# Kernel tuning notes

Hardware: AMD Instinct MI355X
Metric: run time of the kernel (lower is better)

## Reference

```python
import jax, jax.numpy as jnp
import numpy as np

N = 50000
E = 600000


def gcn_conv(x, W, b, src, dst, n):
    # PyG GCNConv: h = x @ W; add self-loops; symmetric normalization; aggregate; + bias
    h = x @ W  # [N, out]
    deg = jnp.zeros((n,), h.dtype).at[dst].add(1.0) + 1.0  # self-loop included
    dinv = jax.lax.rsqrt(deg)  # deg >= 1, always finite
    coef = dinv[src] * dinv[dst]  # [E]
    msg = h[src] * coef[:, None]  # [E, out]  (the memory-bound gather)
    agg = jax.ops.segment_sum(msg, dst, num_segments=n)
    agg = agg + h * (dinv * dinv)[:, None]  # self-loop contribution
    return agg + b


def setup_inputs() -> dict:
    key = jax.random.key(0)
    ks = jax.random.split(key, 8)
    x = jax.random.normal(ks[0], (N, 128), dtype=jnp.float32)
    edge_index = jax.random.randint(ks[1], (2, E), 0, N, dtype=jnp.int64 if jax.config.jax_enable_x64 else jnp.int32)
    def glorot(k, fan_in, fan_out):
        s = jnp.sqrt(6.0 / (fan_in + fan_out))
        return jax.random.uniform(k, (fan_in, fan_out), jnp.float32, -s, s)
    W1 = glorot(ks[2], 128, 128)
    b1 = jnp.zeros((128,), jnp.float32)
    W2 = glorot(ks[3], 128, 64)
    b2 = jnp.zeros((64,), jnp.float32)
    W3 = glorot(ks[4], 64, 16)
    b3 = jnp.zeros((16,), jnp.float32)
    return {"x": x, "edge_index": edge_index, "W1": W1, "b1": b1, "W2": W2, "b2": b2, "W3": W3, "b3": b3}


def reference(x, edge_index, W1, b1, W2, b2, W3, b3):
    src, dst = edge_index[0], edge_index[1]
    n = x.shape[0]
    h = jax.nn.relu(gcn_conv(x, W1, b1, src, dst, n))
    h = jax.nn.relu(gcn_conv(h, W2, b2, src, dst, n))
    h = gcn_conv(h, W3, b3, src, dst, n)
    return h
```

## Files before the change

### kernel.cpp

```cpp
#include <hip/hip_runtime.h>
#include <hip/hip_fp16.h>
#include <type_traits>


typedef _Float16 f16x8 __attribute__((ext_vector_type(8)));
typedef float f32x4 __attribute__((ext_vector_type(4)));

#define CSR_CAP 32

__device__ inline float2 h2f(unsigned int u) {
  __half2 h = __builtin_bit_cast(__half2, u);
  return __half22float2(h);
}

__device__ inline void fma8h(float4& a0, float4& a1, const uint4& g, float w) {
  float2 f0 = h2f(g.x), f1 = h2f(g.y), f2 = h2f(g.z), f3 = h2f(g.w);
  a0.x = fmaf(f0.x, w, a0.x);
  a0.y = fmaf(f0.y, w, a0.y);
  a0.z = fmaf(f1.x, w, a0.z);
  a0.w = fmaf(f1.y, w, a0.w);
  a1.x = fmaf(f2.x, w, a1.x);
  a1.y = fmaf(f2.y, w, a1.y);
  a1.z = fmaf(f3.x, w, a1.z);
  a1.w = fmaf(f3.y, w, a1.w);
}

__device__ inline void add8h(float4& a0, float4& a1, const uint4& g) {
  float2 f0 = h2f(g.x), f1 = h2f(g.y), f2 = h2f(g.z), f3 = h2f(g.w);
  a0.x += f0.x; a0.y += f0.y; a0.z += f1.x; a0.w += f1.y;
  a1.x += f2.x; a1.y += f2.y; a1.z += f3.x; a1.w += f3.y;
}

__device__ inline unsigned int pack2h(float x, float y) {
  __half2 h = __floats2half2_rn(x, y);
  return __builtin_bit_cast(unsigned int, h);
}

__device__ inline uint2 pack4h(const float4& v) {
  uint2 r;
  r.x = pack2h(v.x, v.y);
  r.y = pack2h(v.z, v.w);
  return r;
}

template <int K, int F, typename TIN>
__global__ __launch_bounds__(512) void gemm_mfma(const TIN* __restrict__ A,
                                                 const float* __restrict__ W,
                                                 __half* __restrict__ C16, int n,
                                                 int nwaves,
                                                 const int* __restrict__ src,
                                                 const int* __restrict__ dst,
                                                 int* __restrict__ cur,
                                                 unsigned short* __restrict__ csr,
                                                 int E) {
  constexpr int KP = K + 8;
  constexpr int KS = K / 32;
  constexpr int NT = F / 16;

  __shared__ __half Ws[F * KP];

  int t = threadIdx.x;

  if (t >= 256) {
    __syncthreads();
    int base = blockIdx.x * 256 + (t - 256);
    int stride = gridDim.x * 256;
    for (int e0 = base; e0 < E; e0 += 4 * stride) {
      int d[4], s[4];
      bool v[4];
#pragma unroll
      for (int u = 0; u < 4; ++u) {
        int e = e0 + u * stride;
        v[u] = e < E;
        int ee = v[u] ? e : 0;
        d[u] = dst[ee];
        s[u] = src[ee];
      }
      int pos[4];
#pragma unroll
      for (int u = 0; u < 4; ++u)
        if (v[u]) pos[u] = atomicAdd(&cur[d[u]], 1);
#pragma unroll
      for (int u = 0; u < 4; ++u)
        if (v[u]) {
          int p = pos[u] >= CSR_CAP ? CSR_CAP - 1 : pos[u];
          csr[(size_t)d[u] * CSR_CAP + p] = (unsigned short)s[u];
        }
    }
    return;
  }

  for (int i = t; i < K * F; i += 256) {
    int kk = i / F, nn = i % F;
    Ws[nn * KP + kk] = __float2half(W[i]);
  }
  __syncthreads();

  int wave = blockIdx.x * 4 + (t >> 6);
  if (wave >= nwaves) return;
  int lane = t & 63;
  int m = lane & 15;
  int quad = lane >> 4;

  int arow = wave * 16 + m;
  if (arow >= n) arow = n - 1;

  f16x8 af[KS];
  if constexpr (std::is_same_v<TIN, float>) {
#pragma unroll
    for (int ks = 0; ks < KS; ++ks) {
      const float* p = A + (size_t)arow * K + ks * 32 + quad * 8;
      float4 lo = *(const float4*)p;
      float4 hi = *(const float4*)(p + 4);
      f16x8 a;
      a[0] = (_Float16)lo.x; a[1] = (_Float16)lo.y;
      a[2] = (_Float16)lo.z; a[3] = (_Float16)lo.w;
      a[4] = (_Float16)hi.x; a[5] = (_Float16)hi.y;
      a[6] = (_Float16)hi.z; a[7] = (_Float16)hi.w;
      af[ks] = a;
    }
  } else {
#pragma unroll
    for (int ks = 0; ks < KS; ++ks)
      af[ks] = *(const f16x8*)(const void*)&A[(size_t)arow * K + ks * 32 + quad * 8];
  }

  f32x4 acc[NT];
#pragma unroll
  for (int nt = 0; nt < NT; ++nt) acc[nt] = (f32x4){0.f, 0.f, 0.f, 0.f};
#pragma unroll
  for (int nt = 0; nt < NT; ++nt)
#pragma unroll
    for (int ks = 0; ks < KS; ++ks) {
      f16x8 b = *(const f16x8*)(const void*)&Ws[(nt * 16 + m) * KP + ks * 32 + quad * 8];
      acc[nt] = __builtin_amdgcn_mfma_f32_16x16x32_f16(af[ks], b, acc[nt], 0, 0, 0);
    }

  int rbase = wave * 16 + quad * 4;
#pragma unroll
  for (int nt = 0; nt < NT; ++nt)
#pragma unroll
    for (int r = 0; r < 4; ++r) {
      int rr = rbase + r;
      if (rr < n) C16[(size_t)rr * F + nt * 16 + m] = __float2half(acc[nt][r]);
    }
}

template <int K, int F, int CPL, int EU, bool PRE, bool SCOUT>
__global__ __launch_bounds__(512) void aggmm(
    const __half* __restrict__ hprev, const float* __restrict__ W,
    const float* __restrict__ bias, const int* __restrict__ cnt,
    const unsigned short* __restrict__ csr, __half* __restrict__ C16, int n) {
  constexpr int KP = K + 8;
  constexpr int KS = K / 32;
  constexpr int NT = F / 16;
  constexpr int RS = K / 8;
  static_assert(8 * CPL == RS, "chunk coverage (8 chunk-lanes per half)");

  __shared__ __half Ws[F * KP];
  __shared__ __half As[32 * KP];

  int t = threadIdx.x;
  for (int i = t; i < K * F; i += 512) {
    int kk = i / F, nn = i % F;
    Ws[nn * KP + kk] = __float2half(W[i]);
  }

  int wid = t >> 6;
  int lane = t & 63;
  int nb = blockIdx.x * 32;

  {
    int ng = lane >> 4;
    int sl = lane & 15;
    int half = sl >> 3;
    int fl = sl & 7;
    int nib = wid * 4 + ng;
    int node = nb + nib;
    int nd = node < n ? node : n - 1;
    const uint4* h4 = (const uint4*)hprev;
    int c0 = cnt[nd];
    float di = rsqrtf((float)c0 + 1.0f);
    int cc = c0 < CSR_CAP ? c0 : CSR_CAP;
    float4 acc[CPL][2];
#pragma unroll
    for (int c = 0; c < CPL; ++c) {
      acc[c][0] = make_float4(0.f, 0.f, 0.f, 0.f);
      acc[c][1] = make_float4(0.f, 0.f, 0.f, 0.f);
    }
    if (half == 0) {
#pragma unroll
      for (int c = 0; c < CPL; ++c) {
        uint4 sv = h4[(size_t)nd * RS + fl + c * 8];
        if constexpr (PRE)
          add8h(acc[c][0], acc[c][1], sv);
        else
          fma8h(acc[c][0], acc[c][1], sv, di * di);
      }
    }
    int j0 = nd * CSR_CAP;
    int e = j0 + cc;
    int j = j0 + half;
    int p[EU];
#pragma unroll
    for (int u = 0; u < EU; ++u) p[u] = csr[j + 2 * u];
    for (; j + 2 * EU - 2 < e;) {
      uint4 g[EU][CPL];
#pragma unroll
      for (int u = 0; u < EU; ++u)
#pragma unroll
        for (int c = 0; c < CPL; ++c) g[u][c] = h4[(size_t)p[u] * RS + fl + c * 8];
      int cs[EU];
      if constexpr (!PRE) {
#pragma unroll
        for (int u = 0; u < EU; ++u) cs[u] = cnt[p[u]];
      }
      j += 2 * EU;
      int pn[EU];
#pragma unroll
      for (int u = 0; u < EU; ++u) pn[u] = csr[j + 2 * u];
#pragma unroll
      for (int u = 0; u < EU; ++u) {
        if constexpr (PRE) {
#pragma unroll
          for (int c = 0; c < CPL; ++c) add8h(acc[c][0], acc[c][1], g[u][c]);
        } else {
          float w = rsqrtf((float)cs[u] + 1.0f) * di;
#pragma unroll
          for (int c = 0; c < CPL; ++c) fma8h(acc[c][0], acc[c][1], g[u][c], w);
        }
      }
#pragma unroll
      for (int u = 0; u < EU; ++u) p[u] = pn[u];
    }
#pragma unroll
    for (int u = 0; u < EU; ++u) {
      if (j + 2 * u < e) {
        if constexpr (PRE) {
#pragma unroll
          for (int c = 0; c < CPL; ++c) {
            uint4 g = h4[(size_t)p[u] * RS + fl + c * 8];
            add8h(acc[c][0], acc[c][1], g);
          }
        } else {
          float w = rsqrtf((float)cnt[p[u]] + 1.0f) * di;
#pragma unroll
          for (int c = 0; c < CPL; ++c) {
            uint4 g = h4[(size_t)p[u] * RS + fl + c * 8];
            fma8h(acc[c][0], acc[c][1], g, w);
          }
        }
      }
    }
#pragma unroll
    for (int c = 0; c < CPL; ++c) {
      acc[c][0].x += __shfl_xor(acc[c][0].x, 8);
      acc[c][0].y += __shfl_xor(acc[c][0].y, 8);
      acc[c][0].z += __shfl_xor(acc[c][0].z, 8);
      acc[c][0].w += __shfl_xor(acc[c][0].w, 8);
      acc[c][1].x += __shfl_xor(acc[c][1].x, 8);
      acc[c][1].y += __shfl_xor(acc[c][1].y, 8);
      acc[c][1].z += __shfl_xor(acc[c][1].z, 8);
      acc[c][1].w += __shfl_xor(acc[c][1].w, 8);
    }
    if (half == 0) {
      float sc = PRE ? di : 1.0f;
#pragma unroll
      for (int c = 0; c < CPL; ++c) {
        int ch = fl + c * 8;
        float4 b0 = *(const float4*)&bias[ch * 8];
        float4 b1 = *(const float4*)&bias[ch * 8 + 4];
        float4 r0 = make_float4(fmaxf(acc[c][0].x * sc + b0.x, 0.f),
                                fmaxf(acc[c][0].y * sc + b0.y, 0.f),
                                fmaxf(acc[c][0].z * sc + b0.z, 0.f),
                                fmaxf(acc[c][0].w * sc + b0.w, 0.f));
        float4 r1 = make_float4(fmaxf(acc[c][1].x * sc + b1.x, 0.f),
                                fmaxf(acc[c][1].y * sc + b1.y, 0.f),
                                fmaxf(acc[c][1].z * sc + b1.z, 0.f),
                                fmaxf(acc[c][1].w * sc + b1.w, 0.f));
        uint2 lo = pack4h(r0), hi = pack4h(r1);
        uint4 pk;
        pk.x = lo.x; pk.y = lo.y; pk.z = hi.x; pk.w = hi.y;
        *(uint4*)&As[(size_t)nib * KP + ch * 8] = pk;
      }
    }
  }

  __syncthreads();

  if (wid < 2) {
    int m = lane & 15;
    int quad = lane >> 4;
    const __half* At = &As[(size_t)wid * 16 * KP];
    f16x8 af[KS];
#pragma unroll
    for (int ks = 0; ks < KS; ++ks)
      af[ks] = *(const f16x8*)(const void*)&At[m * KP + ks * 32 + quad * 8];

    f32x4 acc2[NT];
#pragma unroll
    for (int nt = 0; nt < NT; ++nt) acc2[nt] = (f32x4){0.f, 0.f, 0.f, 0.f};
#pragma unroll
    for (int nt = 0; nt < NT; ++nt)
#pragma unroll
      for (int ks = 0; ks < KS; ++ks) {
        f16x8 bfr = *(const f16x8*)(const void*)&Ws[(nt * 16 + m) * KP + ks * 32 + quad * 8];
        acc2[nt] = __builtin_amdgcn_mfma_f32_16x16x32_f16(af[ks], bfr, acc2[nt], 0, 0, 0);
      }

    int rbase = nb + wid * 16 + quad * 4;
    float rw[4];
#pragma unroll
    for (int r = 0; r < 4; ++r) {
      if constexpr (SCOUT) {
        int rr = rbase + r;
        int rc = rr < n ? rr : n - 1;
        rw[r] = rsqrtf((float)cnt[rc] + 1.0f);
      } else {
        rw[r] = 1.0f;
      }
    }
#pragma unroll
    for (int nt = 0; nt < NT; ++nt)
#pragma unroll
      for (int r = 0; r < 4; ++r) {
        int rr = rbase + r;
        if (rr < n) C16[(size_t)rr * F + nt * 16 + m] = __float2half(acc2[nt][r] * rw[r]);
      }
  }
}

__global__ __launch_bounds__(256) void agg_final(
    const __half* __restrict__ h16, const int* __restrict__ cnt,
    const unsigned short* __restrict__ csr, const float* __restrict__ bias,
    float* __restrict__ out, int n) {
  int node = blockIdx.x * 64 + threadIdx.x / 4;
  int q = threadIdx.x & 3;
  int half = q >> 1;
  int fl = q & 1;
  bool valid = node < n;
  int nd = valid ? node : n - 1;

  const uint4* h4 = (const uint4*)h16;
  int c0 = cnt[nd];
  float di = rsqrtf((float)c0 + 1.0f);
  int cc = c0 < CSR_CAP ? c0 : CSR_CAP;
  float4 a0 = make_float4(0.f, 0.f, 0.f, 0.f);
  float4 a1 = make_float4(0.f, 0.f, 0.f, 0.f);
  if (half == 0) {
    uint4 sv = h4[(size_t)nd * 2 + fl];
    add8h(a0, a1, sv);
  }
  int s = nd * CSR_CAP;
  int e = s + cc;
  int j = s + half;
  for (; j + 2 < e; j += 4) {
    int p0 = csr[j];
    int p1 = csr[j + 2];
    uint4 g0 = h4[(size_t)p0 * 2 + fl];
    uint4 g1 = h4[(size_t)p1 * 2 + fl];
    add8h(a0, a1, g0);
    add8h(a0, a1, g1);
  }
  for (; j < e; j += 2) {
    int p = csr[j];
    uint4 g = h4[(size_t)p * 2 + fl];
    add8h(a0, a1, g);
  }

  a0.x += __shfl_xor(a0.x, 2);
  a0.y += __shfl_xor(a0.y, 2);
  a0.z += __shfl_xor(a0.z, 2);
  a0.w += __shfl_xor(a0.w, 2);
  a1.x += __shfl_xor(a1.x, 2);
  a1.y += __shfl_xor(a1.y, 2);
  a1.z += __shfl_xor(a1.z, 2);
  a1.w += __shfl_xor(a1.w, 2);

  if (valid && half == 0) {
    float4 b0 = *(const float4*)&bias[fl * 8];
    float4 b1 = *(const float4*)&bias[fl * 8 + 4];
    float4 r0 = make_float4(a0.x * di + b0.x, a0.y * di + b0.y,
                            a0.z * di + b0.z, a0.w * di + b0.w);
    float4 r1 = make_float4(a1.x * di + b1.x, a1.y * di + b1.y,
                            a1.z * di + b1.z, a1.w * di + b1.w);
    float* op = &out[(size_t)node * 16 + fl * 8];
    *(float4*)op = r0;
    *(float4*)(op + 4) = r1;
  }
}


extern "C" void kernel_launch(void* const* d_in, const int* in_sizes, int n_in,
                              void* d_out, int out_size, void* d_ws, size_t ws_size,
                              hipStream_t stream) {
  const float* x = (const float*)d_in[0];
  const int* edge = (const int*)d_in[1];
  const float* W1 = (const float*)d_in[2];
  const float* b1 = (const float*)d_in[3];
  const float* W2 = (const float*)d_in[4];
  const float* b2 = (const float*)d_in[5];
  const float* W3 = (const float*)d_in[6];
  const float* b3 = (const float*)d_in[7];

  const int N = in_sizes[0] / 128;
  const int E = in_sizes[1] / 2;
  const int* src = edge;
  const int* dstp = edge + E;
  float* out = (float*)d_out;

  size_t off = 0;
  auto take = [&](size_t bytes) -> void* {
    void* r = (char*)d_ws + off;
    off += (bytes + 255) & ~(size_t)255;
    return r;
  };
  int* cur = (int*)take((size_t)N * 4);
  unsigned short* csr =
      (unsigned short*)take((size_t)N * CSR_CAP * 2 + 256);
  __half* t1 = (__half*)take((size_t)N * 128 * 2);
  __half* t2 = (__half*)take((size_t)N * 64 * 2);
  __half* t3 = (__half*)take((size_t)N * 16 * 2);

  hipMemsetAsync(d_ws, 0, ((size_t)N * 4 + 255) & ~(size_t)255, stream);

  int nwaves = (N + 15) / 16;
  int gblk = (nwaves + 3) / 4;
  int ablk = (N + 31) / 32;
  int fblk = (N + 63) / 64;

  gemm_mfma<128, 128, float><<<gblk, 512, 0, stream>>>(x, W1, t1, N, nwaves,
                                                       src, dstp, cur, csr, E);

  aggmm<128, 64, 2, 4, false, true><<<ablk, 512, 0, stream>>>(t1, W2, b1, cur, csr, t2, N);
  aggmm<64, 16, 1, 4, true, true><<<ablk, 512, 0, stream>>>(t2, W3, b2, cur, csr, t3, N);
  agg_final<<<fblk, 256, 0, stream>>>(t3, cur, csr, b3, out, N);
}
```

Baseline: 175.7 us.

## Process 64 nodes per block with 8 lanes per node and column passes

Each aggregation block now handles 64 nodes instead of 32. Each node gets 8 lanes instead of 16, so every lane walks the neighbour list in several sequential 32-column passes rather than holding all columns at once. Four waves run the MFMA epilogue instead of two, and the grid is halved. This cuts per-lane register pressure and raises concurrent nodes per wave, but the CSR indices and degree counts are now reread on every pass, and each gather covers fewer columns.

Result: slower. 186.5 us (+6.1%).

```diff
diff --git a/kernel.cpp b/kernel.cpp
--- a/kernel.cpp
+++ b/kernel.cpp
@@ -146,7 +146,7 @@
     }
 }
 
-template <int K, int F, int CPL, int EU, bool PRE, bool SCOUT>
+template <int K, int F, int P, int EU, bool PRE, bool SCOUT>
 __global__ __launch_bounds__(512) void aggmm(
     const __half* __restrict__ hprev, const float* __restrict__ W,
     const float* __restrict__ bias, const int* __restrict__ cnt,
@@ -155,10 +155,10 @@
   constexpr int KS = K / 32;
   constexpr int NT = F / 16;
   constexpr int RS = K / 8;
-  static_assert(8 * CPL == RS, "chunk coverage (8 chunk-lanes per half)");
+  static_assert(P * 32 == K, "chunk coverage (32 cols per pass)");
 
   __shared__ __half Ws[F * KP];
-  __shared__ __half As[32 * KP];
+  __shared__ __half As[64 * KP];
 
   int t = threadIdx.x;
   for (int i = t; i < K * F; i += 512) {
@@ -168,127 +168,108 @@
 
   int wid = t >> 6;
   int lane = t & 63;
-  int nb = blockIdx.x * 32;
+  int nb = blockIdx.x * 64;
 
   {
-    int ng = lane >> 4;
-    int sl = lane & 15;
-    int half = sl >> 3;
-    int fl = sl & 7;
-    int nib = wid * 4 + ng;
+    int ng = lane >> 3;
+    int sl = lane & 7;
+    int half = sl >> 2;
+    int fl = sl & 3;
+    int nib = wid * 8 + ng;
     int node = nb + nib;
     int nd = node < n ? node : n - 1;
     const uint4* h4 = (const uint4*)hprev;
     int c0 = cnt[nd];
     float di = rsqrtf((float)c0 + 1.0f);
     int cc = c0 < CSR_CAP ? c0 : CSR_CAP;
-    float4 acc[CPL][2];
-#pragma unroll
-    for (int c = 0; c < CPL; ++c) {
-      acc[c][0] = make_float4(0.f, 0.f, 0.f, 0.f);
-      acc[c][1] = make_float4(0.f, 0.f, 0.f, 0.f);
-    }
-    if (half == 0) {
-#pragma unroll
-      for (int c = 0; c < CPL; ++c) {
-        uint4 sv = h4[(size_t)nd * RS + fl + c * 8];
-        if constexpr (PRE)
-          add8h(acc[c][0], acc[c][1], sv);
-        else
-          fma8h(acc[c][0], acc[c][1], sv, di * di);
-      }
-    }
     int j0 = nd * CSR_CAP;
     int e = j0 + cc;
-    int j = j0 + half;
-    int p[EU];
-#pragma unroll
-    for (int u = 0; u < EU; ++u) p[u] = csr[j + 2 * u];
-    for (; j + 2 * EU - 2 < e;) {
-      uint4 g[EU][CPL];
-#pragma unroll
-      for (int u = 0; u < EU; ++u)
-#pragma unroll
-        for (int c = 0; c < CPL; ++c) g[u][c] = h4[(size_t)p[u] * RS + fl + c * 8];
-      int cs[EU];
-      if constexpr (!PRE) {
-#pragma unroll
-        for (int u = 0; u < EU; ++u) cs[u] = cnt[p[u]];
-      }
-      j += 2 * EU;
-      int pn[EU];
-#pragma unroll
-      for (int u = 0; u < EU; ++u) pn[u] = csr[j + 2 * u];
-#pragma unroll
-      for (int u = 0; u < EU; ++u) {
-        if constexpr (PRE) {
-#pragma unroll
-          for (int c = 0; c < CPL; ++c) add8h(acc[c][0], acc[c][1], g[u][c]);
-        } else {
-          float w = rsqrtf((float)cs[u] + 1.0f) * di;
-#pragma unroll
-          for (int c = 0; c < CPL; ++c) fma8h(acc[c][0], acc[c][1], g[u][c], w);
+
+#pragma unroll 1
+    for (int ph = 0; ph < P; ++ph) {
+      int cb = ph * 4 + fl;
+      float4 a0 = make_float4(0.f, 0.f, 0.f, 0.f);
+      float4 a1 = make_float4(0.f, 0.f, 0.f, 0.f);
+      if (half == 0) {
+        uint4 sv = h4[(size_t)nd * RS + cb];
+        if constexpr (PRE)
+          add8h(a0, a1, sv);
+        else
+          fma8h(a0, a1, sv, di * di);
+      }
+      int j = j0 + half;
+      int p[EU];
+#pragma unroll
+      for (int u = 0; u < EU; ++u) p[u] = csr[j + 2 * u];
+      for (; j + 2 * EU - 2 < e;) {
+        uint4 g[EU];
+#pragma unroll
+        for (int u = 0; u < EU; ++u) g[u] = h4[(size_t)p[u] * RS + cb];
+        int cs[EU];
+        if constexpr (!PRE) {
+#pragma unroll
+          for (int u = 0; u < EU; ++u) cs[u] = cnt[p[u]];
         }
-      }
-#pragma unroll
-      for (int u = 0; u < EU; ++u) p[u] = pn[u];
-    }
-#pragma unroll
-    for (int u = 0; u < EU; ++u) {
-      if (j + 2 * u < e) {
-        if constexpr (PRE) {
-#pragma unroll
-          for (int c = 0; c < CPL; ++c) {
-            uint4 g = h4[(size_t)p[u] * RS + fl + c * 8];
-            add8h(acc[c][0], acc[c][1], g);
-          }
-        } else {
-          float w = rsqrtf((float)cnt[p[u]] + 1.0f) * di;
-#pragma unroll
-          for (int c = 0; c < CPL; ++c) {
-            uint4 g = h4[(size_t)p[u] * RS + fl + c * 8];
-            fma8h(acc[c][0], acc[c][1], g, w);
+        j += 2 * EU;
+        int pn[EU];
+#pragma unroll
+        for (int u = 0; u < EU; ++u) pn[u] = csr[j + 2 * u];
+#pragma unroll
+        for (int u = 0; u < EU; ++u) {
+          if constexpr (PRE) {
+            add8h(a0, a1, g[u]);
+          } else {
+            float w = rsqrtf((float)cs[u] + 1.0f) * di;
+            fma8h(a0, a1, g[u], w);
           }
         }
-      }
-    }
-#pragma unroll
-    for (int c = 0; c < CPL; ++c) {
-      acc[c][0].x += __shfl_xor(acc[c][0].x, 8);
-      acc[c][0].y += __shfl_xor(acc[c][0].y, 8);
-      acc[c][0].z += __shfl_xor(acc[c][0].z, 8);
-      acc[c][0].w += __shfl_xor(acc[c][0].w, 8);
-      acc[c][1].x += __shfl_xor(acc[c][1].x, 8);
-      acc[c][1].y += __shfl_xor(acc[c][1].y, 8);
-      acc[c][1].z += __shfl_xor(acc[c][1].z, 8);
-      acc[c][1].w += __shfl_xor(acc[c][1].w, 8);
-    }
-    if (half == 0) {
-      float sc = PRE ? di : 1.0f;
-#pragma unroll
-      for (int c = 0; c < CPL; ++c) {
-        int ch = fl + c * 8;
-        float4 b0 = *(const float4*)&bias[ch * 8];
-        float4 b1 = *(const float4*)&bias[ch * 8 + 4];
-        float4 r0 = make_float4(fmaxf(acc[c][0].x * sc + b0.x, 0.f),
-                                fmaxf(acc[c][0].y * sc + b0.y, 0.f),
-                                fmaxf(acc[c][0].z * sc + b0.z, 0.f),
-                                fmaxf(acc[c][0].w * sc + b0.w, 0.f));
-        float4 r1 = make_float4(fmaxf(acc[c][1].x * sc + b1.x, 0.f),
-                                fmaxf(acc[c][1].y * sc + b1.y, 0.f),
-                                fmaxf(acc[c][1].z * sc + b1.z, 0.f),
-                                fmaxf(acc[c][1].w * sc + b1.w, 0.f));
+#pragma unroll
+        for (int u = 0; u < EU; ++u) p[u] = pn[u];
+      }
+#pragma unroll
+      for (int u = 0; u < EU; ++u) {
+        if (j + 2 * u < e) {
+          uint4 g = h4[(size_t)p[u] * RS + cb];
+          if constexpr (PRE) {
+            add8h(a0, a1, g);
+          } else {
+            float w = rsqrtf((float)cnt[p[u]] + 1.0f) * di;
+            fma8h(a0, a1, g, w);
+          }
+        }
+      }
+      a0.x += __shfl_xor(a0.x, 4);
+      a0.y += __shfl_xor(a0.y, 4);
+      a0.z += __shfl_xor(a0.z, 4);
+      a0.w += __shfl_xor(a0.w, 4);
+      a1.x += __shfl_xor(a1.x, 4);
+      a1.y += __shfl_xor(a1.y, 4);
+      a1.z += __shfl_xor(a1.z, 4);
+      a1.w += __shfl_xor(a1.w, 4);
+      if (half == 0) {
+        float sc = PRE ? di : 1.0f;
+        int ch0 = ph * 32 + fl * 8;
+        float4 b0 = *(const float4*)&bias[ch0];
+        float4 b1 = *(const float4*)&bias[ch0 + 4];
+        float4 r0 = make_float4(fmaxf(a0.x * sc + b0.x, 0.f),
+                                fmaxf(a0.y * sc + b0.y, 0.f),
+                                fmaxf(a0.z * sc + b0.z, 0.f),
+                                fmaxf(a0.w * sc + b0.w, 0.f));
+        float4 r1 = make_float4(fmaxf(a1.x * sc + b1.x, 0.f),
+                                fmaxf(a1.y * sc + b1.y, 0.f),
+                                fmaxf(a1.z * sc + b1.z, 0.f),
+                                fmaxf(a1.w * sc + b1.w, 0.f));
         uint2 lo = pack4h(r0), hi = pack4h(r1);
         uint4 pk;
         pk.x = lo.x; pk.y = lo.y; pk.z = hi.x; pk.w = hi.y;
-        *(uint4*)&As[(size_t)nib * KP + ch * 8] = pk;
+        *(uint4*)&As[(size_t)nib * KP + ch0] = pk;
       }
     }
   }
 
   __syncthreads();
 
-  if (wid < 2) {
+  if (wid < 4) {
     int m = lane & 15;
     int quad = lane >> 4;
     const __half* At = &As[(size_t)wid * 16 * KP];
@@ -426,13 +407,12 @@
 
   int nwaves = (N + 15) / 16;
   int gblk = (nwaves + 3) / 4;
-  int ablk = (N + 31) / 32;
   int fblk = (N + 63) / 64;
 
   gemm_mfma<128, 128, float><<<gblk, 512, 0, stream>>>(x, W1, t1, N, nwaves,
                                                        src, dstp, cur, csr, E);
 
-  aggmm<128, 64, 2, 4, false, true><<<ablk, 512, 0, stream>>>(t1, W2, b1, cur, csr, t2, N);
-  aggmm<64, 16, 1, 4, true, true><<<ablk, 512, 0, stream>>>(t2, W3, b2, cur, csr, t3, N);
+  aggmm<128, 64, 4, 4, false, true><<<fblk, 512, 0, stream>>>(t1, W2, b1, cur, csr, t2, N);
+  aggmm<64, 16, 2, 4, true, true><<<fblk, 512, 0, stream>>>(t2, W3, b2, cur, csr, t3, N);
   agg_final<<<fblk, 256, 0, stream>>>(t3, cur, csr, b3, out, N);
 }
```
